# Optimization experiments

Measured on AMD Instinct MI355X. Metric: run time of the kernel, lower is better.

Reference implementation:

```python
import jax, jax.numpy as jnp
import numpy as np

N = 8192      # total nodes (32 graphs x 256 nodes)
B = 32        # graphs in batch
E = 65536     # edges per graph (avg degree 16)
DK = 512      # d_k = d_v
H = 32        # mlp / conv channel width
VB = 2048     # body visual dim
VF = 512      # face visual dim
EPS = 1e-5


def setup_inputs() -> dict:
    key = jax.random.key(0)
    ks = jax.random.split(key, 26)
    def n(k, sh, s=1.0):
        return jax.random.normal(k, sh, dtype=jnp.float32) * s
    s2, s512, s32 = 1.0 / np.sqrt(2.0), 1.0 / np.sqrt(512.0), 1.0 / np.sqrt(32.0)
    inp = {}
    inp["x"] = n(ks[0], (N, 2))
    inp["visual_body"] = n(ks[1], (N, VB))
    inp["visual_face"] = n(ks[2], (N, VF))
    # attention projections (no bias)
    inp["Wq"] = n(ks[3], (2, DK), s2)
    inp["Wk"] = n(ks[4], (2, DK), s2)
    inp["Wv"] = n(ks[5], (2, DK), s2)
    # input_mlp: LayerNorm(512) -> PReLU -> Linear(512,32)
    inp["ln_g"] = jnp.ones((DK,), jnp.float32)
    inp["ln_b"] = jnp.zeros((DK,), jnp.float32)
    inp["prelu_a"] = jnp.float32(0.25)
    inp["mlp_W"] = n(ks[6], (DK, H), s512)
    inp["mlp_b"] = jnp.zeros((H,), jnp.float32)
    # node projection Linear(32,1)
    inp["np_W"] = n(ks[7], (H, 1), s32)
    inp["np_b"] = jnp.zeros((1,), jnp.float32)
    # CMCosConv linear weights (32->32) for body / face
    inp["body_W"] = n(ks[8], (H, H), s32)
    inp["body_b"] = jnp.zeros((H,), jnp.float32)
    inp["face_W"] = n(ks[9], (H, H), s32)
    inp["face_b"] = jnp.zeros((H,), jnp.float32)
    # gcn projections Linear(32,1)
    inp["pb_W"] = n(ks[10], (H, 1), s32)
    inp["pb_b"] = jnp.zeros((1,), jnp.float32)
    inp["pf_W"] = n(ks[11], (H, 1), s32)
    inp["pf_b"] = jnp.zeros((1,), jnp.float32)
    # int-valued graph structure
    inp["edge_index_body"] = jax.random.randint(ks[12], (2, E), 0, N)
    inp["edge_index_face"] = jax.random.randint(ks[13], (2, E), 0, N)
    inp["batch_vec"] = jnp.arange(N, dtype=jnp.int64) // (N // B)  # 32 graphs, 256 nodes each
    return inp


def cmcos_conv(x, edge_index, visual, W, b):
    # per-edge cosine(visual_src, visual_dst) * Linear(x_src), scatter-sum to dst
    src, dst = edge_index[0], edge_index[1]
    h = x @ W + b                                          # [N, H]
    vn = visual * jax.lax.rsqrt(jnp.sum(visual * visual, -1, keepdims=True) + 1e-8)
    w = jnp.sum(vn[src] * vn[dst], axis=-1)                # [E] cosine edge weights
    msg = w[:, None] * h[src]                              # [E, H]
    return jax.ops.segment_sum(msg, dst, num_segments=x.shape[0])


def reference(x, visual_body, visual_face, Wq, Wk, Wv, ln_g, ln_b, prelu_a,
              mlp_W, mlp_b, np_W, np_b, body_W, body_b, face_W, face_b,
              pb_W, pb_b, pf_W, pf_b, edge_index_body, edge_index_face, batch_vec):
    sz_b = int(batch_vec[-1]) + 1
    q = (x @ Wq).reshape(sz_b, -1, DK)
    k = (x @ Wk).reshape(sz_b, -1, DK)
    v = (x @ Wv).reshape(sz_b, -1, DK)
    attn = jax.nn.softmax(jnp.einsum('bqd,bkd->bqk', q, k) / np.sqrt(DK), axis=-1)
    out = jnp.einsum('bqk,bkd->bqd', attn, v).reshape(-1, DK)   # [N, 512]
    # input_mlp: LayerNorm -> PReLU -> Linear (dropout is identity in eval)
    mu = jnp.mean(out, -1, keepdims=True)
    var = jnp.mean((out - mu) ** 2, -1, keepdims=True)
    h = (out - mu) * jax.lax.rsqrt(var + EPS) * ln_g + ln_b
    h = jnp.where(h >= 0, h, prelu_a * h)
    h = h @ mlp_W + mlp_b                                       # [N, 32]
    nodes_scores = (h @ np_W + np_b)[:, 0]
    hb = cmcos_conv(h, edge_index_body, visual_body, body_W, body_b)
    hf = cmcos_conv(h, edge_index_face, visual_face, face_W, face_b)
    gcn_scores_body = (hb @ pb_W + pb_b)[:, 0]
    gcn_scores_face = (hf @ pf_W + pf_b)[:, 0]
    return nodes_scores + gcn_scores_body + gcn_scores_face
```

## Files before the change

### kernel.cpp

```cpp
#include <hip/hip_runtime.h>

#define NN 8192
#define NB 32
#define NG 256
#define NE 65536
#define DK 512
#define HC 32
#define DB 2048
#define DF 512

#define BODY_DW (NN*DB/4)
#define FACE_DW (NN*DF/4)
#define B_BODY (BODY_DW/2048)
#define B_FACE (FACE_DW/2048)

typedef float v2f __attribute__((ext_vector_type(2)));

#if __has_builtin(__builtin_amdgcn_cvt_pk_f32_fp8) && __has_builtin(__builtin_amdgcn_cvt_pk_fp8_f32)
#define HW_FP8 1
#else
#define HW_FP8 0
#endif

__device__ __forceinline__ float fp8_dec(unsigned u) {
    unsigned e = (u >> 3) & 15u, m = u & 7u, s = u & 0x80u;
    float v = e ? __uint_as_float(((e + 120u) << 23) | (m << 20))
                : (float)m * 0.001953125f;
    return s ? -v : v;
}
__device__ __forceinline__ unsigned fp8_enc(float x) {
    unsigned sb = (__float_as_uint(x) >> 24) & 0x80u;
    float a = fabsf(x);
    if (a >= 448.f) return sb | 0x7Eu;
    if (a < 0.015625f) {
        int c = (int)rintf(a * 512.f);
        if (c > 7) return sb | 0x08u;
        return sb | (unsigned)c;
    }
    int ex; (void)frexpf(a, &ex);
    float p = ldexpf(a, 1 - ex);
    int m = (int)rintf((p - 1.f) * 8.f);
    int e = ex - 1 + 7;
    if (m == 8) { m = 0; e++; }
    if (e >= 16) return sb | 0x7Eu;
    return sb | (unsigned)(e << 3) | (unsigned)m;
}
__device__ __forceinline__ unsigned pack4_fp8(float x, float y, float z, float w) {
#if HW_FP8
    int u = __builtin_amdgcn_cvt_pk_fp8_f32(x, y, 0, false);
    u = __builtin_amdgcn_cvt_pk_fp8_f32(z, w, u, true);
    return (unsigned)u;
#else
    return fp8_enc(x) | (fp8_enc(y) << 8) | (fp8_enc(z) << 16) | (fp8_enc(w) << 24);
#endif
}
__device__ __forceinline__ float fp8dot4(unsigned a, unsigned b) {
#if HW_FP8
    v2f al = __builtin_amdgcn_cvt_pk_f32_fp8((int)a, false);
    v2f ah = __builtin_amdgcn_cvt_pk_f32_fp8((int)a, true);
    v2f bl = __builtin_amdgcn_cvt_pk_f32_fp8((int)b, false);
    v2f bh = __builtin_amdgcn_cvt_pk_f32_fp8((int)b, true);
    return al.x*bl.x + al.y*bl.y + ah.x*bh.x + ah.y*bh.y;
#else
    float s = 0.f;
    #pragma unroll
    for (int j = 0; j < 4; j++)
        s += fp8_dec((a >> (8*j)) & 255u) * fp8_dec((b >> (8*j)) & 255u);
    return s;
#endif
}
__device__ __forceinline__ float fp8dot16(int4 a, int4 b) {
    return fp8dot4((unsigned)a.x, (unsigned)b.x) + fp8dot4((unsigned)a.y, (unsigned)b.y)
         + fp8dot4((unsigned)a.z, (unsigned)b.z) + fp8dot4((unsigned)a.w, (unsigned)b.w);
}
__device__ __forceinline__ float d4(float4 v) {
    return v.x*v.x + v.y*v.y + v.z*v.z + v.w*v.w;
}

struct Params {
    const float *vb, *vf, *x, *Wq, *Wk, *Wv, *ln_g, *ln_b, *prelu_a;
    const float *mlp_W, *mlp_b, *np_W, *np_b, *body_W, *body_b, *face_W, *face_b;
    const float *pb_W, *pb_b, *pf_W, *pf_b;
    const int *eib, *eif;
    unsigned *vnb, *vnf;
    float *invb, *invf;
    float *a_ws, *sb, *sf, *fused;
    float *out;
};

__global__ __launch_bounds__(256, 4) void k1_kernel(Params p) {
    __shared__ float2 xs[NG];
    __shared__ float pm[4][4];
    __shared__ float sm4[4];
    __shared__ float rss[16];
    const int bid = blockIdx.x, tid = threadIdx.x;
    const int lane = tid & 63, wave = tid >> 6;

    if (bid < B_BODY + B_FACE) {
        const bool body = bid < B_BODY;
        const float4* __restrict__ src = body ? (const float4*)p.vb : (const float4*)p.vf;
        unsigned* __restrict__ dst = body ? p.vnb : p.vnf;
        const int base = (body ? bid : bid - B_BODY) * 2048 + tid;
        if (tid < 16) rss[tid] = 0.f;
        __syncthreads();
        float4 v0 = src[base];
        float4 v1 = src[base + 256];
        float4 v2 = src[base + 512];
        float4 v3 = src[base + 768];
        float4 v4 = src[base + 1024];
        float4 v5 = src[base + 1280];
        float4 v6 = src[base + 1536];
        float4 v7 = src[base + 1792];
        dst[base]        = pack4_fp8(v0.x, v0.y, v0.z, v0.w);
        dst[base + 256]  = pack4_fp8(v1.x, v1.y, v1.z, v1.w);
        dst[base + 512]  = pack4_fp8(v2.x, v2.y, v2.z, v2.w);
        dst[base + 768]  = pack4_fp8(v3.x, v3.y, v3.z, v3.w);
        dst[base + 1024] = pack4_fp8(v4.x, v4.y, v4.z, v4.w);
        dst[base + 1280] = pack4_fp8(v5.x, v5.y, v5.z, v5.w);
        dst[base + 1536] = pack4_fp8(v6.x, v6.y, v6.z, v6.w);
        dst[base + 1792] = pack4_fp8(v7.x, v7.y, v7.z, v7.w);
        if (body) {
            float sq[4];
            sq[0] = d4(v0) + d4(v1);
            sq[1] = d4(v2) + d4(v3);
            sq[2] = d4(v4) + d4(v5);
            sq[3] = d4(v6) + d4(v7);
            #pragma unroll
            for (int r = 0; r < 4; r++) {
                float ss = sq[r];
                #pragma unroll
                for (int off = 32; off > 0; off >>= 1) ss += __shfl_xor(ss, off);
                if (lane == 0) atomicAdd(&rss[r], ss);
            }
            __syncthreads();
            if (tid < 4) p.invb[bid*4 + tid] = rsqrtf(rss[tid] + 1e-8f);
        } else {
            float sq[8] = {d4(v0), d4(v1), d4(v2), d4(v3), d4(v4), d4(v5), d4(v6), d4(v7)};
            #pragma unroll
            for (int j = 0; j < 8; j++) {
                float ss = sq[j];
                #pragma unroll
                for (int off = 32; off > 0; off >>= 1) ss += __shfl_xor(ss, off);
                if (lane == 0) atomicAdd(&rss[(wave >> 1) + 2*j], ss);
            }
            __syncthreads();
            if (tid < 16) p.invf[(bid - B_BODY)*16 + tid] = rsqrtf(rss[tid] + 1e-8f);
        }
        return;
    }
    if (bid < B_BODY + B_FACE + NB) {
        const int gg = bid - (B_BODY + B_FACE);
        xs[tid] = ((const float2*)p.x)[gg*NG + tid];
        const int d = tid * 2;
        float q0a = p.Wq[d],    q0b = p.Wq[d+1];
        float q1a = p.Wq[DK+d], q1b = p.Wq[DK+d+1];
        float k0a = p.Wk[d],    k0b = p.Wk[d+1];
        float k1a = p.Wk[DK+d], k1b = p.Wk[DK+d+1];
        float m00 = q0a*k0a + q0b*k0b;
        float m01 = q0a*k1a + q0b*k1b;
        float m10 = q1a*k0a + q1b*k0b;
        float m11 = q1a*k1a + q1b*k1b;
        #pragma unroll
        for (int off = 32; off > 0; off >>= 1) {
            m00 += __shfl_down(m00,off); m01 += __shfl_down(m01,off);
            m10 += __shfl_down(m10,off); m11 += __shfl_down(m11,off);
        }
        if (lane == 0) { pm[wave][0]=m00; pm[wave][1]=m01; pm[wave][2]=m10; pm[wave][3]=m11; }
        __syncthreads();
        if (tid < 4) sm4[tid] = pm[0][tid] + pm[1][tid] + pm[2][tid] + pm[3][tid];
        __syncthreads();
        const float scale = 0.04419417382415922f;
        const float2 xi = xs[tid];
        const float u0 = (xi.x*sm4[0] + xi.y*sm4[2]) * scale;
        const float u1 = (xi.x*sm4[1] + xi.y*sm4[3]) * scale;
        float m = -1e30f;
        for (int j = 0; j < NG; j++) m = fmaxf(m, u0*xs[j].x + u1*xs[j].y);
        float S = 0.f, a0 = 0.f, a1 = 0.f;
        for (int j = 0; j < NG; j++) {
            float2 xj = xs[j];
            float pr = __expf(u0*xj.x + u1*xj.y - m);
            S += pr; a0 += pr*xj.x; a1 += pr*xj.y;
        }
        const float invS = 1.f / S;
        ((float2*)p.a_ws)[gg*NG + tid] = make_float2(a0*invS, a1*invS);
        return;
    }
    if (tid < HC) {
        float s = 0.f;
        #pragma unroll 8
        for (int c = 0; c < HC; c++) s += p.body_W[tid*HC + c] * p.pb_W[c];
        p.fused[tid] = s;
    } else if (tid < 2*HC) {
        const int cp = tid - HC;
        float s = 0.f;
        #pragma unroll 8
        for (int c = 0; c < HC; c++) s += p.face_W[cp*HC + c] * p.pf_W[c];
        p.fused[HC + cp] = s;
    } else if (tid == 2*HC) {
        float s = 0.f;
        for (int c = 0; c < HC; c++) s += p.body_b[c] * p.pb_W[c];
        p.fused[64] = s;
    } else if (tid == 2*HC + 1) {
        float s = 0.f;
        for (int c = 0; c < HC; c++) s += p.face_b[c] * p.pf_W[c];
        p.fused[65] = s;
    }
}

__global__ __launch_bounds__(256) void k2_kernel(Params p) {
    __shared__ float t[4][DK];
    const int tid = threadIdx.x;
    const int wave = tid >> 6, lane = tid & 63;
    const int node = blockIdx.x * 4 + wave;

    const float a0 = p.a_ws[node*2], a1 = p.a_ws[node*2+1];
    const float4* wv0 = (const float4*)p.Wv;
    const float4* wv1 = (const float4*)(p.Wv + DK);
    const float4* g4 = (const float4*)p.ln_g;
    const float4* b4 = (const float4*)p.ln_b;
    float4 W0[2], W1[2], Gg[2], Bb[2];
    #pragma unroll
    for (int k = 0; k < 2; k++) {
        int c4 = lane*2 + k;
        W0[k] = wv0[c4]; W1[k] = wv1[c4]; Gg[k] = g4[c4]; Bb[k] = b4[c4];
    }
    float s0=0.f, s1=0.f, q00=0.f, q01=0.f, q11=0.f;
    #pragma unroll
    for (int k = 0; k < 2; k++) {
        const float* u = (const float*)&W0[k];
        const float* v = (const float*)&W1[k];
        #pragma unroll
        for (int j = 0; j < 4; j++) {
            s0 += u[j]; s1 += v[j];
            q00 += u[j]*u[j]; q01 += u[j]*v[j]; q11 += v[j]*v[j];
        }
    }
    #pragma unroll
    for (int off = 1; off < 64; off <<= 1) {
        s0 += __shfl_xor(s0,off); s1 += __shfl_xor(s1,off);
        q00 += __shfl_xor(q00,off); q01 += __shfl_xor(q01,off); q11 += __shfl_xor(q11,off);
    }
    const float mean = (a0*s0 + a1*s1) * (1.f/DK);
    const float msq  = (a0*a0*q00 + 2.f*a0*a1*q01 + a1*a1*q11) * (1.f/DK);
    const float inv  = rsqrtf(msq - mean*mean + 1e-5f);
    const float alpha = p.prelu_a[0];
    #pragma unroll
    for (int k = 0; k < 2; k++) {
        int c4 = lane*2 + k;
        const float* u = (const float*)&W0[k];
        const float* v = (const float*)&W1[k];
        const float* gf = (const float*)&Gg[k];
        const float* bf = (const float*)&Bb[k];
        #pragma unroll
        for (int j = 0; j < 4; j++) {
            float od = a0*u[j] + a1*v[j];
            float nd = (od - mean) * inv * gf[j] + bf[j];
            t[wave][c4*4 + j] = (nd >= 0.f) ? nd : alpha*nd;
        }
    }
    __syncthreads();
    const int c = lane & 31, half = lane >> 5;
    const float* tp = t[wave] + half*256;
    const float* mw = p.mlp_W + half*256*HC + c;
    float p0=0.f, p1=0.f, p2=0.f, p3=0.f;
    #pragma unroll 4
    for (int d = 0; d < 256; d += 4) {
        p0 += tp[d]   * mw[d*HC];
        p1 += tp[d+1] * mw[(d+1)*HC];
        p2 += tp[d+2] * mw[(d+2)*HC];
        p3 += tp[d+3] * mw[(d+3)*HC];
    }
    float partl = (p0+p1) + (p2+p3);
    partl += __shfl_down(partl, 32);
    float v0 = 0.f, v1 = 0.f, v2 = 0.f;
    if (lane < 32) {
        float hc = partl + p.mlp_b[c];
        v0 = hc * p.np_W[c];
        v1 = hc * p.fused[c];
        v2 = hc * p.fused[HC + c];
    }
    #pragma unroll
    for (int off = 16; off > 0; off >>= 1) {
        v0 += __shfl_down(v0, off);
        v1 += __shfl_down(v1, off);
        v2 += __shfl_down(v2, off);
    }
    if (lane == 0) {
        p.out[node] = v0 + p.np_b[0] + p.pb_b[0] + p.pf_b[0];
        p.sb[node] = v1 + p.fused[64];
        p.sf[node] = v2 + p.fused[65];
    }
}

__global__ __launch_bounds__(256) void scat_kernel(Params p) {
    const int wave = threadIdx.x >> 6, lane = threadIdx.x & 63;
    if (blockIdx.x < NE/8) {
        const int e = blockIdx.x * 8 + wave * 2;
        const int sA = p.eib[e],     dA = p.eib[NE + e];
        const int sB = p.eib[e + 1], dB = p.eib[NE + e + 1];
        const int4* ap0 = (const int4*)(p.vnb + (size_t)sA * (DB/4));
        const int4* bp0 = (const int4*)(p.vnb + (size_t)dA * (DB/4));
        const int4* ap1 = (const int4*)(p.vnb + (size_t)sB * (DB/4));
        const int4* bp1 = (const int4*)(p.vnb + (size_t)dB * (DB/4));
        int4 a00 = ap0[lane], a01 = ap0[lane + 64];
        int4 b00 = bp0[lane], b01 = bp0[lane + 64];
        int4 a10 = ap1[lane], a11 = ap1[lane + 64];
        int4 b10 = bp1[lane], b11 = bp1[lane + 64];
        float x0 = fp8dot16(a00, b00) + fp8dot16(a01, b01);
        float x1 = fp8dot16(a10, b10) + fp8dot16(a11, b11);
        #pragma unroll
        for (int off = 32; off > 0; off >>= 1) {
            x0 += __shfl_xor(x0, off);
            x1 += __shfl_xor(x1, off);
        }
        if (lane == 0) {
            atomicAdd(&p.out[dA], x0 * p.invb[sA] * p.invb[dA] * p.sb[sA]);
            atomicAdd(&p.out[dB], x1 * p.invb[sB] * p.invb[dB] * p.sb[sB]);
        }
    } else {
        const int e = (blockIdx.x - NE/8) * 16 + wave * 4;
        const int s0 = p.eif[e],     d0 = p.eif[NE + e];
        const int s1 = p.eif[e + 1], d1 = p.eif[NE + e + 1];
        const int s2 = p.eif[e + 2], d2 = p.eif[NE + e + 2];
        const int s3 = p.eif[e + 3], d3 = p.eif[NE + e + 3];
        const int2* ap0 = (const int2*)(p.vnf + (size_t)s0 * (DF/4));
        const int2* bp0 = (const int2*)(p.vnf + (size_t)d0 * (DF/4));
        const int2* ap1 = (const int2*)(p.vnf + (size_t)s1 * (DF/4));
        const int2* bp1 = (const int2*)(p.vnf + (size_t)d1 * (DF/4));
        const int2* ap2 = (const int2*)(p.vnf + (size_t)s2 * (DF/4));
        const int2* bp2 = (const int2*)(p.vnf + (size_t)d2 * (DF/4));
        const int2* ap3 = (const int2*)(p.vnf + (size_t)s3 * (DF/4));
        const int2* bp3 = (const int2*)(p.vnf + (size_t)d3 * (DF/4));
        int2 a0 = ap0[lane], b0 = bp0[lane];
        int2 a1 = ap1[lane], b1 = bp1[lane];
        int2 a2 = ap2[lane], b2 = bp2[lane];
        int2 a3 = ap3[lane], b3 = bp3[lane];
        float x0 = fp8dot4((unsigned)a0.x,(unsigned)b0.x) + fp8dot4((unsigned)a0.y,(unsigned)b0.y);
        float x1 = fp8dot4((unsigned)a1.x,(unsigned)b1.x) + fp8dot4((unsigned)a1.y,(unsigned)b1.y);
        float x2 = fp8dot4((unsigned)a2.x,(unsigned)b2.x) + fp8dot4((unsigned)a2.y,(unsigned)b2.y);
        float x3 = fp8dot4((unsigned)a3.x,(unsigned)b3.x) + fp8dot4((unsigned)a3.y,(unsigned)b3.y);
        #pragma unroll
        for (int off = 32; off > 0; off >>= 1) {
            x0 += __shfl_xor(x0, off);
            x1 += __shfl_xor(x1, off);
            x2 += __shfl_xor(x2, off);
            x3 += __shfl_xor(x3, off);
        }
        if (lane == 0) {
            atomicAdd(&p.out[d0], x0 * p.invf[s0] * p.invf[d0] * p.sf[s0]);
            atomicAdd(&p.out[d1], x1 * p.invf[s1] * p.invf[d1] * p.sf[s1]);
            atomicAdd(&p.out[d2], x2 * p.invf[s2] * p.invf[d2] * p.sf[s2]);
            atomicAdd(&p.out[d3], x3 * p.invf[s3] * p.invf[d3] * p.sf[s3]);
        }
    }
}

extern "C" void kernel_launch(void* const* d_in, const int* in_sizes, int n_in,
                              void* d_out, int out_size, void* d_ws, size_t ws_size,
                              hipStream_t stream) {
    char* ws = (char*)d_ws;
    size_t off = 0;
    auto alloc = [&](size_t bytes) { void* pp = ws + off; off += (bytes + 15) & ~size_t(15); return pp; };

    Params p;
    p.vb      = (const float*)d_in[1];
    p.vf      = (const float*)d_in[2];
    p.x       = (const float*)d_in[0];
    p.Wq      = (const float*)d_in[3];
    p.Wk      = (const float*)d_in[4];
    p.Wv      = (const float*)d_in[5];
    p.ln_g    = (const float*)d_in[6];
    p.ln_b    = (const float*)d_in[7];
    p.prelu_a = (const float*)d_in[8];
    p.mlp_W   = (const float*)d_in[9];
    p.mlp_b   = (const float*)d_in[10];
    p.np_W    = (const float*)d_in[11];
    p.np_b    = (const float*)d_in[12];
    p.body_W  = (const float*)d_in[13];
    p.body_b  = (const float*)d_in[14];
    p.face_W  = (const float*)d_in[15];
    p.face_b  = (const float*)d_in[16];
    p.pb_W    = (const float*)d_in[17];
    p.pb_b    = (const float*)d_in[18];
    p.pf_W    = (const float*)d_in[19];
    p.pf_b    = (const float*)d_in[20];
    p.eib     = (const int*)d_in[21];
    p.eif     = (const int*)d_in[22];
    p.vnb     = (unsigned*)alloc((size_t)BODY_DW*4);
    p.vnf     = (unsigned*)alloc((size_t)FACE_DW*4);
    p.invb    = (float*)alloc((size_t)NN*4);
    p.invf    = (float*)alloc((size_t)NN*4);
    p.a_ws    = (float*)alloc((size_t)NN*2*4);
    p.sb      = (float*)alloc((size_t)NN*4);
    p.sf      = (float*)alloc((size_t)NN*4);
    p.fused   = (float*)alloc((size_t)66*4);
    p.out     = (float*)d_out;

    k1_kernel<<<B_BODY + B_FACE + NB + 1, 256, 0, stream>>>(p);
    k2_kernel<<<NN/4, 256, 0, stream>>>(p);
    scat_kernel<<<NE/8 + NE/16, 256, 0, stream>>>(p);
}
```

Measured before the change: 222.5 us.

## Switch cosine features to int8 sdot4 and fold MLP weights into projection vectors

Visual features are now quantised to int8 with a fixed scale of 16 instead of fp8, and the per-edge cosine dot products use the integer sdot4 instruction instead of unpacking fp8 to float. The k2 MLP is collapsed algebraically: mlp_W is premultiplied by the node, body and face projection vectors in k1, so each node needs only three 512-long dot products instead of a 512x32 matmul through shared memory. The Wv statistics for LayerNorm are reduced once in k1 rather than in every k2 block, and the small blocks are placed first in the grid. The fixed int8 scale with clamping assumes the feature magnitudes suit that range, so accuracy depends on the input distribution, and the unscaling is folded into sb/sf.

```diff
diff --git a/kernel.cpp b/kernel.cpp
--- a/kernel.cpp
+++ b/kernel.cpp
@@ -13,68 +13,52 @@
 #define FACE_DW (NN*DF/4)
 #define B_BODY (BODY_DW/2048)
 #define B_FACE (FACE_DW/2048)
-
-typedef float v2f __attribute__((ext_vector_type(2)));
-
-#if __has_builtin(__builtin_amdgcn_cvt_pk_f32_fp8) && __has_builtin(__builtin_amdgcn_cvt_pk_fp8_f32)
-#define HW_FP8 1
+#define QSCALE 16.0f
+
+typedef float v4f __attribute__((ext_vector_type(4)));
+
+#if __has_builtin(__builtin_amdgcn_sdot4)
+#define HW_SDOT 1
 #else
-#define HW_FP8 0
+#define HW_SDOT 0
 #endif
 
-__device__ __forceinline__ float fp8_dec(unsigned u) {
-    unsigned e = (u >> 3) & 15u, m = u & 7u, s = u & 0x80u;
-    float v = e ? __uint_as_float(((e + 120u) << 23) | (m << 20))
-                : (float)m * 0.001953125f;
-    return s ? -v : v;
-}
-__device__ __forceinline__ unsigned fp8_enc(float x) {
-    unsigned sb = (__float_as_uint(x) >> 24) & 0x80u;
-    float a = fabsf(x);
-    if (a >= 448.f) return sb | 0x7Eu;
-    if (a < 0.015625f) {
-        int c = (int)rintf(a * 512.f);
-        if (c > 7) return sb | 0x08u;
-        return sb | (unsigned)c;
-    }
-    int ex; (void)frexpf(a, &ex);
-    float p = ldexpf(a, 1 - ex);
-    int m = (int)rintf((p - 1.f) * 8.f);
-    int e = ex - 1 + 7;
-    if (m == 8) { m = 0; e++; }
-    if (e >= 16) return sb | 0x7Eu;
-    return sb | (unsigned)(e << 3) | (unsigned)m;
-}
-__device__ __forceinline__ unsigned pack4_fp8(float x, float y, float z, float w) {
-#if HW_FP8
-    int u = __builtin_amdgcn_cvt_pk_fp8_f32(x, y, 0, false);
-    u = __builtin_amdgcn_cvt_pk_fp8_f32(z, w, u, true);
-    return (unsigned)u;
+__device__ __forceinline__ unsigned pack4_i8(float4 v) {
+    int i0 = (int)rintf(fmaxf(fminf(v.x * QSCALE, 127.f), -127.f));
+    int i1 = (int)rintf(fmaxf(fminf(v.y * QSCALE, 127.f), -127.f));
+    int i2 = (int)rintf(fmaxf(fminf(v.z * QSCALE, 127.f), -127.f));
+    int i3 = (int)rintf(fmaxf(fminf(v.w * QSCALE, 127.f), -127.f));
+    return (unsigned)(i0 & 255) | ((unsigned)(i1 & 255) << 8)
+         | ((unsigned)(i2 & 255) << 16) | ((unsigned)(i3 & 255) << 24);
+}
+__device__ __forceinline__ int sdot4(int a, int b, int c) {
+#if HW_SDOT
+    return __builtin_amdgcn_sdot4(a, b, c, false);
 #else
-    return fp8_enc(x) | (fp8_enc(y) << 8) | (fp8_enc(z) << 16) | (fp8_enc(w) << 24);
+    c += (int)(signed char)(a)       * (int)(signed char)(b);
+    c += (int)(signed char)(a >> 8)  * (int)(signed char)(b >> 8);
+    c += (int)(signed char)(a >> 16) * (int)(signed char)(b >> 16);
+    c += (int)(signed char)(a >> 24) * (int)(signed char)(b >> 24);
+    return c;
 #endif
 }
-__device__ __forceinline__ float fp8dot4(unsigned a, unsigned b) {
-#if HW_FP8
-    v2f al = __builtin_amdgcn_cvt_pk_f32_fp8((int)a, false);
-    v2f ah = __builtin_amdgcn_cvt_pk_f32_fp8((int)a, true);
-    v2f bl = __builtin_amdgcn_cvt_pk_f32_fp8((int)b, false);
-    v2f bh = __builtin_amdgcn_cvt_pk_f32_fp8((int)b, true);
-    return al.x*bl.x + al.y*bl.y + ah.x*bh.x + ah.y*bh.y;
-#else
-    float s = 0.f;
-    #pragma unroll
-    for (int j = 0; j < 4; j++)
-        s += fp8_dec((a >> (8*j)) & 255u) * fp8_dec((b >> (8*j)) & 255u);
-    return s;
-#endif
-}
-__device__ __forceinline__ float fp8dot16(int4 a, int4 b) {
-    return fp8dot4((unsigned)a.x, (unsigned)b.x) + fp8dot4((unsigned)a.y, (unsigned)b.y)
-         + fp8dot4((unsigned)a.z, (unsigned)b.z) + fp8dot4((unsigned)a.w, (unsigned)b.w);
+__device__ __forceinline__ int dot16(int4 a, int4 b, int c) {
+    c = sdot4(a.x, b.x, c);
+    c = sdot4(a.y, b.y, c);
+    c = sdot4(a.z, b.z, c);
+    c = sdot4(a.w, b.w, c);
+    return c;
 }
 __device__ __forceinline__ float d4(float4 v) {
     return v.x*v.x + v.y*v.y + v.z*v.z + v.w*v.w;
+}
+__device__ __forceinline__ v4f prelu4(v4f nd, float alpha) {
+    v4f r;
+    r.x = (nd.x >= 0.f) ? nd.x : alpha*nd.x;
+    r.y = (nd.y >= 0.f) ? nd.y : alpha*nd.y;
+    r.z = (nd.z >= 0.f) ? nd.z : alpha*nd.z;
+    r.w = (nd.w >= 0.f) ? nd.w : alpha*nd.w;
+    return r;
 }
 
 struct Params {
@@ -85,71 +69,22 @@
     unsigned *vnb, *vnf;
     float *invb, *invf;
     float *a_ws, *sb, *sf, *fused;
+    float *mvec;
     float *out;
 };
 
-__global__ __launch_bounds__(256, 4) void k1_kernel(Params p) {
+__global__ __launch_bounds__(256) void k1_kernel(Params p) {
     __shared__ float2 xs[NG];
     __shared__ float pm[4][4];
     __shared__ float sm4[4];
     __shared__ float rss[16];
+    __shared__ float wred[4][8];
+    __shared__ float fs_np[HC], fs_fb[HC], fs_ff[HC];
     const int bid = blockIdx.x, tid = threadIdx.x;
     const int lane = tid & 63, wave = tid >> 6;
 
-    if (bid < B_BODY + B_FACE) {
-        const bool body = bid < B_BODY;
-        const float4* __restrict__ src = body ? (const float4*)p.vb : (const float4*)p.vf;
-        unsigned* __restrict__ dst = body ? p.vnb : p.vnf;
-        const int base = (body ? bid : bid - B_BODY) * 2048 + tid;
-        if (tid < 16) rss[tid] = 0.f;
-        __syncthreads();
-        float4 v0 = src[base];
-        float4 v1 = src[base + 256];
-        float4 v2 = src[base + 512];
-        float4 v3 = src[base + 768];
-        float4 v4 = src[base + 1024];
-        float4 v5 = src[base + 1280];
-        float4 v6 = src[base + 1536];
-        float4 v7 = src[base + 1792];
-        dst[base]        = pack4_fp8(v0.x, v0.y, v0.z, v0.w);
-        dst[base + 256]  = pack4_fp8(v1.x, v1.y, v1.z, v1.w);
-        dst[base + 512]  = pack4_fp8(v2.x, v2.y, v2.z, v2.w);
-        dst[base + 768]  = pack4_fp8(v3.x, v3.y, v3.z, v3.w);
-        dst[base + 1024] = pack4_fp8(v4.x, v4.y, v4.z, v4.w);
-        dst[base + 1280] = pack4_fp8(v5.x, v5.y, v5.z, v5.w);
-        dst[base + 1536] = pack4_fp8(v6.x, v6.y, v6.z, v6.w);
-        dst[base + 1792] = pack4_fp8(v7.x, v7.y, v7.z, v7.w);
-        if (body) {
-            float sq[4];
-            sq[0] = d4(v0) + d4(v1);
-            sq[1] = d4(v2) + d4(v3);
-            sq[2] = d4(v4) + d4(v5);
-            sq[3] = d4(v6) + d4(v7);
-            #pragma unroll
-            for (int r = 0; r < 4; r++) {
-                float ss = sq[r];
-                #pragma unroll
-                for (int off = 32; off > 0; off >>= 1) ss += __shfl_xor(ss, off);
-                if (lane == 0) atomicAdd(&rss[r], ss);
-            }
-            __syncthreads();
-            if (tid < 4) p.invb[bid*4 + tid] = rsqrtf(rss[tid] + 1e-8f);
-        } else {
-            float sq[8] = {d4(v0), d4(v1), d4(v2), d4(v3), d4(v4), d4(v5), d4(v6), d4(v7)};
-            #pragma unroll
-            for (int j = 0; j < 8; j++) {
-                float ss = sq[j];
-                #pragma unroll
-                for (int off = 32; off > 0; off >>= 1) ss += __shfl_xor(ss, off);
-                if (lane == 0) atomicAdd(&rss[(wave >> 1) + 2*j], ss);
-            }
-            __syncthreads();
-            if (tid < 16) p.invf[(bid - B_BODY)*16 + tid] = rsqrtf(rss[tid] + 1e-8f);
-        }
-        return;
-    }
-    if (bid < B_BODY + B_FACE + NB) {
-        const int gg = bid - (B_BODY + B_FACE);
+    if (bid < NB) {
+        const int gg = bid;
         xs[tid] = ((const float2*)p.x)[gg*NG + tid];
         const int d = tid * 2;
         float q0a = p.Wq[d],    q0b = p.Wq[d+1];
@@ -185,110 +120,158 @@
         ((float2*)p.a_ws)[gg*NG + tid] = make_float2(a0*invS, a1*invS);
         return;
     }
-    if (tid < HC) {
-        float s = 0.f;
-        #pragma unroll 8
-        for (int c = 0; c < HC; c++) s += p.body_W[tid*HC + c] * p.pb_W[c];
-        p.fused[tid] = s;
-    } else if (tid < 2*HC) {
-        const int cp = tid - HC;
-        float s = 0.f;
-        #pragma unroll 8
-        for (int c = 0; c < HC; c++) s += p.face_W[cp*HC + c] * p.pf_W[c];
-        p.fused[HC + cp] = s;
-    } else if (tid == 2*HC) {
-        float s = 0.f;
-        for (int c = 0; c < HC; c++) s += p.body_b[c] * p.pb_W[c];
-        p.fused[64] = s;
-    } else if (tid == 2*HC + 1) {
-        float s = 0.f;
-        for (int c = 0; c < HC; c++) s += p.face_b[c] * p.pf_W[c];
-        p.fused[65] = s;
+    if (bid == NB) {
+        {
+            const int d = tid * 2;
+            float u0 = p.Wv[d], u1 = p.Wv[d+1];
+            float w0 = p.Wv[DK+d], w1 = p.Wv[DK+d+1];
+            float s0 = u0 + u1, s1 = w0 + w1;
+            float q00 = u0*u0 + u1*u1, q01 = u0*w0 + u1*w1, q11 = w0*w0 + w1*w1;
+            #pragma unroll
+            for (int off = 1; off < 64; off <<= 1) {
+                s0 += __shfl_xor(s0,off); s1 += __shfl_xor(s1,off);
+                q00 += __shfl_xor(q00,off); q01 += __shfl_xor(q01,off); q11 += __shfl_xor(q11,off);
+            }
+            if (lane == 0) {
+                wred[wave][0]=s0; wred[wave][1]=s1; wred[wave][2]=q00; wred[wave][3]=q01; wred[wave][4]=q11;
+            }
+        }
+        if (tid < HC) {
+            float sB = 0.f, sF = 0.f;
+            #pragma unroll 8
+            for (int c = 0; c < HC; c++) {
+                sB += p.body_W[tid*HC + c] * p.pb_W[c];
+                sF += p.face_W[tid*HC + c] * p.pf_W[c];
+            }
+            fs_fb[tid] = sB; fs_ff[tid] = sF;
+            fs_np[tid] = p.np_W[tid];
+        } else if (tid == HC) {
+            float s = 0.f;
+            for (int c = 0; c < HC; c++) s += p.body_b[c] * p.pb_W[c];
+            p.fused[64] = s;
+        } else if (tid == HC + 1) {
+            float s = 0.f;
+            for (int c = 0; c < HC; c++) s += p.face_b[c] * p.pf_W[c];
+            p.fused[65] = s;
+        }
+        __syncthreads();
+        if (tid < 5) p.fused[66+tid] = wred[0][tid]+wred[1][tid]+wred[2][tid]+wred[3][tid];
+        #pragma unroll
+        for (int rr = tid; rr < DK; rr += 256) {
+            const float* row = p.mlp_W + rr*HC;
+            float dnp = 0.f, db = 0.f, df = 0.f;
+            #pragma unroll 8
+            for (int c = 0; c < HC; c++) {
+                float w = row[c];
+                dnp += w * fs_np[c]; db += w * fs_fb[c]; df += w * fs_ff[c];
+            }
+            p.mvec[rr] = dnp; p.mvec[DK + rr] = db; p.mvec[2*DK + rr] = df;
+        }
+        if (tid < 3) {
+            const float* fv = (tid == 0) ? fs_np : (tid == 1) ? fs_fb : fs_ff;
+            float s = 0.f;
+            for (int c = 0; c < HC; c++) s += p.mlp_b[c] * fv[c];
+            p.mvec[3*DK + tid] = s;
+        }
+        return;
+    }
+    {
+        const int pb = bid - (NB + 1);
+        const bool body = pb < B_BODY;
+        const float4* __restrict__ src = body ? (const float4*)p.vb : (const float4*)p.vf;
+        unsigned* __restrict__ dst = body ? p.vnb : p.vnf;
+        const int base = (body ? pb : pb - B_BODY) * 2048 + tid;
+        if (tid < 16) rss[tid] = 0.f;
+        __syncthreads();
+        float4 v0 = src[base];
+        float4 v1 = src[base + 256];
+        float4 v2 = src[base + 512];
+        float4 v3 = src[base + 768];
+        float4 v4 = src[base + 1024];
+        float4 v5 = src[base + 1280];
+        float4 v6 = src[base + 1536];
+        float4 v7 = src[base + 1792];
+        __builtin_amdgcn_sched_barrier(0);
+        dst[base]        = pack4_i8(v0);
+        dst[base + 256]  = pack4_i8(v1);
+        dst[base + 512]  = pack4_i8(v2);
+        dst[base + 768]  = pack4_i8(v3);
+        dst[base + 1024] = pack4_i8(v4);
+        dst[base + 1280] = pack4_i8(v5);
+        dst[base + 1536] = pack4_i8(v6);
+        dst[base + 1792] = pack4_i8(v7);
+        if (body) {
+            float sq[4];
+            sq[0] = d4(v0) + d4(v1);
+            sq[1] = d4(v2) + d4(v3);
+            sq[2] = d4(v4) + d4(v5);
+            sq[3] = d4(v6) + d4(v7);
+            #pragma unroll
+            for (int r = 0; r < 4; r++) {
+                float ss = sq[r];
+                #pragma unroll
+                for (int off = 32; off > 0; off >>= 1) ss += __shfl_xor(ss, off);
+                if (lane == 0) atomicAdd(&rss[r], ss);
+            }
+            __syncthreads();
+            if (tid < 4) p.invb[pb*4 + tid] = rsqrtf(rss[tid] + 1e-8f);
+        } else {
+            float sq[8] = {d4(v0), d4(v1), d4(v2), d4(v3), d4(v4), d4(v5), d4(v6), d4(v7)};
+            #pragma unroll
+            for (int j = 0; j < 8; j++) {
+                float ss = sq[j];
+                #pragma unroll
+                for (int off = 32; off > 0; off >>= 1) ss += __shfl_xor(ss, off);
+                if (lane == 0) atomicAdd(&rss[(wave >> 1) + 2*j], ss);
+            }
+            __syncthreads();
+            if (tid < 16) p.invf[(pb - B_BODY)*16 + tid] = rsqrtf(rss[tid] + 1e-8f);
+        }
     }
 }
 
 __global__ __launch_bounds__(256) void k2_kernel(Params p) {
-    __shared__ float t[4][DK];
     const int tid = threadIdx.x;
     const int wave = tid >> 6, lane = tid & 63;
     const int node = blockIdx.x * 4 + wave;
 
     const float a0 = p.a_ws[node*2], a1 = p.a_ws[node*2+1];
-    const float4* wv0 = (const float4*)p.Wv;
-    const float4* wv1 = (const float4*)(p.Wv + DK);
-    const float4* g4 = (const float4*)p.ln_g;
-    const float4* b4 = (const float4*)p.ln_b;
-    float4 W0[2], W1[2], Gg[2], Bb[2];
-    #pragma unroll
-    for (int k = 0; k < 2; k++) {
-        int c4 = lane*2 + k;
-        W0[k] = wv0[c4]; W1[k] = wv1[c4]; Gg[k] = g4[c4]; Bb[k] = b4[c4];
-    }
-    float s0=0.f, s1=0.f, q00=0.f, q01=0.f, q11=0.f;
-    #pragma unroll
-    for (int k = 0; k < 2; k++) {
-        const float* u = (const float*)&W0[k];
-        const float* v = (const float*)&W1[k];
-        #pragma unroll
-        for (int j = 0; j < 4; j++) {
-            s0 += u[j]; s1 += v[j];
-            q00 += u[j]*u[j]; q01 += u[j]*v[j]; q11 += v[j]*v[j];
-        }
-    }
-    #pragma unroll
-    for (int off = 1; off < 64; off <<= 1) {
-        s0 += __shfl_xor(s0,off); s1 += __shfl_xor(s1,off);
-        q00 += __shfl_xor(q00,off); q01 += __shfl_xor(q01,off); q11 += __shfl_xor(q11,off);
-    }
+    const float s0 = p.fused[66], s1 = p.fused[67];
+    const float q00 = p.fused[68], q01 = p.fused[69], q11 = p.fused[70];
     const float mean = (a0*s0 + a1*s1) * (1.f/DK);
     const float msq  = (a0*a0*q00 + 2.f*a0*a1*q01 + a1*a1*q11) * (1.f/DK);
     const float inv  = rsqrtf(msq - mean*mean + 1e-5f);
     const float alpha = p.prelu_a[0];
+
+    const v4f* wv0 = (const v4f*)p.Wv;
+    const v4f* wv1 = (const v4f*)(p.Wv + DK);
+    const v4f* g4 = (const v4f*)p.ln_g;
+    const v4f* b4 = (const v4f*)p.ln_b;
+    const v4f* mnp = (const v4f*)p.mvec;
+    const v4f* mb  = (const v4f*)(p.mvec + DK);
+    const v4f* mf  = (const v4f*)(p.mvec + 2*DK);
+
+    const int c4 = lane * 2;
+    v4f t0 = prelu4((a0*wv0[c4]   + a1*wv1[c4]   - mean) * inv * g4[c4]   + b4[c4],   alpha);
+    v4f t1 = prelu4((a0*wv0[c4+1] + a1*wv1[c4+1] - mean) * inv * g4[c4+1] + b4[c4+1], alpha);
+
+    v4f q0 = t0*mnp[c4] + t1*mnp[c4+1];
+    v4f q1 = t0*mb[c4]  + t1*mb[c4+1];
+    v4f q2 = t0*mf[c4]  + t1*mf[c4+1];
+    float d0 = (q0.x+q0.y) + (q0.z+q0.w);
+    float d1 = (q1.x+q1.y) + (q1.z+q1.w);
+    float d2 = (q2.x+q2.y) + (q2.z+q2.w);
     #pragma unroll
-    for (int k = 0; k < 2; k++) {
-        int c4 = lane*2 + k;
-        const float* u = (const float*)&W0[k];
-        const float* v = (const float*)&W1[k];
-        const float* gf = (const float*)&Gg[k];
-        const float* bf = (const float*)&Bb[k];
-        #pragma unroll
-        for (int j = 0; j < 4; j++) {
-            float od = a0*u[j] + a1*v[j];
-            float nd = (od - mean) * inv * gf[j] + bf[j];
-            t[wave][c4*4 + j] = (nd >= 0.f) ? nd : alpha*nd;
-        }
-    }
-    __syncthreads();
-    const int c = lane & 31, half = lane >> 5;
-    const float* tp = t[wave] + half*256;
-    const float* mw = p.mlp_W + half*256*HC + c;
-    float p0=0.f, p1=0.f, p2=0.f, p3=0.f;
-    #pragma unroll 4
-    for (int d = 0; d < 256; d += 4) {
-        p0 += tp[d]   * mw[d*HC];
-        p1 += tp[d+1] * mw[(d+1)*HC];
-        p2 += tp[d+2] * mw[(d+2)*HC];
-        p3 += tp[d+3] * mw[(d+3)*HC];
-    }
-    float partl = (p0+p1) + (p2+p3);
-    partl += __shfl_down(partl, 32);
-    float v0 = 0.f, v1 = 0.f, v2 = 0.f;
-    if (lane < 32) {
-        float hc = partl + p.mlp_b[c];
-        v0 = hc * p.np_W[c];
-        v1 = hc * p.fused[c];
-        v2 = hc * p.fused[HC + c];
-    }
-    #pragma unroll
-    for (int off = 16; off > 0; off >>= 1) {
-        v0 += __shfl_down(v0, off);
-        v1 += __shfl_down(v1, off);
-        v2 += __shfl_down(v2, off);
+    for (int off = 1; off < 64; off <<= 1) {
+        d0 += __shfl_xor(d0, off);
+        d1 += __shfl_xor(d1, off);
+        d2 += __shfl_xor(d2, off);
     }
     if (lane == 0) {
-        p.out[node] = v0 + p.np_b[0] + p.pb_b[0] + p.pf_b[0];
-        p.sb[node] = v1 + p.fused[64];
-        p.sf[node] = v2 + p.fused[65];
+        const float qinv2 = 1.0f / (QSCALE * QSCALE);
+        p.out[node] = d0 + p.mvec[3*DK] + p.np_b[0] + p.pb_b[0] + p.pf_b[0];
+        p.sb[node] = (d1 + p.mvec[3*DK+1] + p.fused[64]) * qinv2;
+        p.sf[node] = (d2 + p.mvec[3*DK+2] + p.fused[65]) * qinv2;
     }
 }
 
@@ -298,24 +281,24 @@
         const int e = blockIdx.x * 8 + wave * 2;
         const int sA = p.eib[e],     dA = p.eib[NE + e];
         const int sB = p.eib[e + 1], dB = p.eib[NE + e + 1];
-        const int4* ap0 = (const int4*)(p.vnb + (size_t)sA * (DB/4));
-        const int4* bp0 = (const int4*)(p.vnb + (size_t)dA * (DB/4));
-        const int4* ap1 = (const int4*)(p.vnb + (size_t)sB * (DB/4));
-        const int4* bp1 = (const int4*)(p.vnb + (size_t)dB * (DB/4));
-        int4 a00 = ap0[lane], a01 = ap0[lane + 64];
-        int4 b00 = bp0[lane], b01 = bp0[lane + 64];
-        int4 a10 = ap1[lane], a11 = ap1[lane + 64];
-        int4 b10 = bp1[lane], b11 = bp1[lane + 64];
-        float x0 = fp8dot16(a00, b00) + fp8dot16(a01, b01);
-        float x1 = fp8dot16(a10, b10) + fp8dot16(a11, b11);
+        const int4* A0 = (const int4*)(p.vnb + (size_t)sA * (DB/4));
+        const int4* B0 = (const int4*)(p.vnb + (size_t)dA * (DB/4));
+        const int4* A1 = (const int4*)(p.vnb + (size_t)sB * (DB/4));
+        const int4* B1 = (const int4*)(p.vnb + (size_t)dB * (DB/4));
+        int4 a00 = A0[lane], a01 = A0[lane + 64];
+        int4 b00 = B0[lane], b01 = B0[lane + 64];
+        int4 a10 = A1[lane], a11 = A1[lane + 64];
+        int4 b10 = B1[lane], b11 = B1[lane + 64];
+        int x0 = dot16(a01, b01, dot16(a00, b00, 0));
+        int x1 = dot16(a11, b11, dot16(a10, b10, 0));
         #pragma unroll
-        for (int off = 32; off > 0; off >>= 1) {
+        for (int off = 1; off < 64; off <<= 1) {
             x0 += __shfl_xor(x0, off);
             x1 += __shfl_xor(x1, off);
         }
         if (lane == 0) {
-            atomicAdd(&p.out[dA], x0 * p.invb[sA] * p.invb[dA] * p.sb[sA]);
-            atomicAdd(&p.out[dB], x1 * p.invb[sB] * p.invb[dB] * p.sb[sB]);
+            atomicAdd(&p.out[dA], (float)x0 * p.invb[sA] * p.invb[dA] * p.sb[sA]);
+            atomicAdd(&p.out[dB], (float)x1 * p.invb[sB] * p.invb[dB] * p.sb[sB]);
         }
     } else {
         const int e = (blockIdx.x - NE/8) * 16 + wave * 4;
@@ -335,22 +318,22 @@
         int2 a1 = ap1[lane], b1 = bp1[lane];
         int2 a2 = ap2[lane], b2 = bp2[lane];
         int2 a3 = ap3[lane], b3 = bp3[lane];
-        float x0 = fp8dot4((unsigned)a0.x,(unsigned)b0.x) + fp8dot4((unsigned)a0.y,(unsigned)b0.y);
-        float x1 = fp8dot4((unsigned)a1.x,(unsigned)b1.x) + fp8dot4((unsigned)a1.y,(unsigned)b1.y);
-        float x2 = fp8dot4((unsigned)a2.x,(unsigned)b2.x) + fp8dot4((unsigned)a2.y,(unsigned)b2.y);
-        float x3 = fp8dot4((unsigned)a3.x,(unsigned)b3.x) + fp8dot4((unsigned)a3.y,(unsigned)b3.y);
+        int x0 = sdot4(a0.y, b0.y, sdot4(a0.x, b0.x, 0));
+        int x1 = sdot4(a1.y, b1.y, sdot4(a1.x, b1.x, 0));
+        int x2 = sdot4(a2.y, b2.y, sdot4(a2.x, b2.x, 0));
+        int x3 = sdot4(a3.y, b3.y, sdot4(a3.x, b3.x, 0));
         #pragma unroll
-        for (int off = 32; off > 0; off >>= 1) {
+        for (int off = 1; off < 64; off <<= 1) {
             x0 += __shfl_xor(x0, off);
             x1 += __shfl_xor(x1, off);
             x2 += __shfl_xor(x2, off);
             x3 += __shfl_xor(x3, off);
         }
         if (lane == 0) {
-            atomicAdd(&p.out[d0], x0 * p.invf[s0] * p.invf[d0] * p.sf[s0]);
-            atomicAdd(&p.out[d1], x1 * p.invf[s1] * p.invf[d1] * p.sf[s1]);
-            atomicAdd(&p.out[d2], x2 * p.invf[s2] * p.invf[d2] * p.sf[s2]);
-            atomicAdd(&p.out[d3], x3 * p.invf[s3] * p.invf[d3] * p.sf[s3]);
+            atomicAdd(&p.out[d0], (float)x0 * p.invf[s0] * p.invf[d0] * p.sf[s0]);
+            atomicAdd(&p.out[d1], (float)x1 * p.invf[s1] * p.invf[d1] * p.sf[s1]);
+            atomicAdd(&p.out[d2], (float)x2 * p.invf[s2] * p.invf[d2] * p.sf[s2]);
+            atomicAdd(&p.out[d3], (float)x3 * p.invf[s3] * p.invf[d3] * p.sf[s3]);
         }
     }
 }
@@ -393,10 +376,11 @@
     p.a_ws    = (float*)alloc((size_t)NN*2*4);
     p.sb      = (float*)alloc((size_t)NN*4);
     p.sf      = (float*)alloc((size_t)NN*4);
-    p.fused   = (float*)alloc((size_t)66*4);
+    p.fused   = (float*)alloc((size_t)72*4);
+    p.mvec    = (float*)alloc((size_t)1544*4);
     p.out     = (float*)d_out;
 
-    k1_kernel<<<B_BODY + B_FACE + NB + 1, 256, 0, stream>>>(p);
+    k1_kernel<<<NB + 1 + B_BODY + B_FACE, 256, 0, stream>>>(p);
     k2_kernel<<<NN/4, 256, 0, stream>>>(p);
     scat_kernel<<<NE/8 + NE/16, 256, 0, stream>>>(p);
 }
```

After: 197.7 us. 11.1% less time.
